# Kernel tuning notes

Measured on AMD Instinct MI355X. Metric: run time of the kernel, lower is better.

## Reference

```python
import jax, jax.numpy as jnp
import numpy as np

N_NODES = 50000

def _gcn_layer(x, src, dst, W, b, n_nodes):
    # x: [N, F_in]; src/dst: [E+N] (self-loops already appended)
    h = x @ W  # [N, F_out]
    deg = jax.ops.segment_sum(jnp.ones_like(dst, dtype=h.dtype), dst, num_segments=n_nodes)
    dinv = jnp.where(deg > 0, jax.lax.rsqrt(deg), 0.0)  # deg^{-1/2}
    norm = dinv[src] * dinv[dst]  # [E+N]
    msg = h[src] * norm[:, None]  # gather + scale
    out = jax.ops.segment_sum(msg, dst, num_segments=n_nodes)  # scatter-add
    return out + b

def setup_inputs() -> dict:
    key = jax.random.key(0)
    k1, k2, k3, k4 = jax.random.split(key, 4)
    d = 128
    E = 800000
    x = jax.random.normal(k1, (N_NODES, d), dtype=jnp.float32)
    edge_index = jax.random.randint(k2, (2, E), 0, N_NODES, dtype=jnp.int64)
    W1 = jax.random.normal(k3, (d, d), dtype=jnp.float32) / np.sqrt(d)
    b1 = jnp.zeros((d,), dtype=jnp.float32)
    W2 = jax.random.normal(k4, (d, d), dtype=jnp.float32) / np.sqrt(d)
    b2 = jnp.zeros((d,), dtype=jnp.float32)
    return {"x": x, "edge_index": edge_index, "W1": W1, "b1": b1, "W2": W2, "b2": b2}

def reference(x, edge_index, W1, b1, W2, b2):
    n = x.shape[0]
    loops = jnp.arange(n, dtype=edge_index.dtype)
    src = jnp.concatenate([edge_index[0], loops])  # add self-loops
    dst = jnp.concatenate([edge_index[1], loops])
    h = _gcn_layer(x, src, dst, W1, b1, n)
    h = jax.nn.relu(h)
    z = _gcn_layer(h, src, dst, W2, b2, n)
    return z
```

## Files before the change

### kernel.cpp

```cpp
#include <hip/hip_runtime.h>
#include <hip/hip_fp16.h>

#define NF 128
#define KC 64
#define NPART 4
#define NPMAX 12544

typedef _Float16 half8  __attribute__((ext_vector_type(8)));
typedef _Float16 half4v __attribute__((ext_vector_type(4)));
typedef float    floatx4 __attribute__((ext_vector_type(4)));

__global__ __launch_bounds__(512) void count2_k(
    const int* __restrict__ dst, unsigned char* __restrict__ pcnt,
    int E, int N, int Ec)
{
    __shared__ int lcnt[NPMAX];
    const int p = blockIdx.x & 3, c = blockIdx.x >> 2;
    const int Np = (N + 3) >> 2;
    const int lo = p * Np, hi = min(lo + Np, N);
    const int sz = hi - lo;
    for (int i = threadIdx.x; i < sz; i += 512) lcnt[i] = 0;
    __syncthreads();

    const int e0 = c * Ec, e1 = min(e0 + Ec, E);
    for (int e = e0 + (int)threadIdx.x * 4; e + 3 < e1; e += 512 * 4) {
        int4 d = *(const int4*)(dst + e);
        if (d.x >= lo && d.x < hi) atomicAdd(&lcnt[d.x - lo], 1);
        if (d.y >= lo && d.y < hi) atomicAdd(&lcnt[d.y - lo], 1);
        if (d.z >= lo && d.z < hi) atomicAdd(&lcnt[d.z - lo], 1);
        if (d.w >= lo && d.w < hi) atomicAdd(&lcnt[d.w - lo], 1);
    }
    int rem0 = e0 + ((e1 - e0) & ~3);
    for (int e = rem0 + (int)threadIdx.x; e < e1; e += 512) {
        int d = dst[e];
        if (d >= lo && d < hi) atomicAdd(&lcnt[d - lo], 1);
    }
    __syncthreads();
    for (int i = threadIdx.x; i < sz; i += 512)
        pcnt[(size_t)c * N + lo + i] = (unsigned char)lcnt[i];
}

__global__ __launch_bounds__(256) void pscan2_k(
    unsigned char* __restrict__ pcnt, float* __restrict__ dinv,
    int* __restrict__ rowptr, int* __restrict__ blocksum, int n, int N, int nb,
    const float* __restrict__ W1, const float* __restrict__ W2,
    __half* __restrict__ WT1, __half* __restrict__ WT2)
{
    if ((int)blockIdx.x >= nb) {
        int idx = ((int)blockIdx.x - nb) * 256 + threadIdx.x;
        const float* W = (idx < 16384) ? W1 : W2;
        __half* WT     = (idx < 16384) ? WT1 : WT2;
        int j = idx & 16383;
        int nn = j & 127, k = j >> 7;
        WT[nn * NF + k] = __float2half(W[k * NF + nn]);
        return;
    }
    __shared__ int sm[256];
    int tid = threadIdx.x;
    int bin = blockIdx.x * 256 + tid;
    int total = 0;
    if (bin < n) {
        #pragma unroll 4
        for (int c = 0; c < KC; c++) {
            size_t o = (size_t)c * N + bin;
            int v = pcnt[o];
            pcnt[o] = (unsigned char)total;
            total += v;
        }
        dinv[bin] = rsqrtf((float)total + 1.0f);
    }
    sm[tid] = total;
    __syncthreads();
    #pragma unroll
    for (int d = 1; d < 256; d <<= 1) {
        int t = (tid >= d) ? sm[tid - d] : 0;
        __syncthreads();
        sm[tid] += t;
        __syncthreads();
    }
    if (bin < n) rowptr[bin] = sm[tid] - total;
    if (tid == 255) blocksum[blockIdx.x] = sm[255];
}

template<bool F32IN>
__device__ __forceinline__ void gemm_body512(
    const void* __restrict__ Xv, const __half* __restrict__ WT,
    const float* __restrict__ dinv, __half* __restrict__ out, int M, int bid,
    __half (*wlds)[136])
{
    const int tid = threadIdx.x;
    {
        int r = tid >> 2;
        int c0 = (tid & 3) * 32;
        const half8* s = (const half8*)(WT + (size_t)r * NF + c0);
        half8* d = (half8*)&wlds[r][c0];
        #pragma unroll
        for (int j = 0; j < 4; j++) d[j] = s[j];
    }
    __syncthreads();

    const int wave = tid >> 6, lane = tid & 63;
    const int quad = lane >> 4, l15 = lane & 15;
    const int rowA = bid * 128 + wave * 16 + l15;
    const int rowc = (rowA < M) ? rowA : (M - 1);

    half8 afr[4];
    if (F32IN) {
        const float* X = (const float*)Xv;
        #pragma unroll
        for (int kc = 0; kc < 4; kc++) {
            const floatx4* p = (const floatx4*)(X + (size_t)rowc * NF + kc * 32 + quad * 8);
            floatx4 u = p[0], v = p[1];
            half8 a;
            a[0] = (_Float16)u[0]; a[1] = (_Float16)u[1];
            a[2] = (_Float16)u[2]; a[3] = (_Float16)u[3];
            a[4] = (_Float16)v[0]; a[5] = (_Float16)v[1];
            a[6] = (_Float16)v[2]; a[7] = (_Float16)v[3];
            afr[kc] = a;
        }
    } else {
        const __half* X = (const __half*)Xv;
        #pragma unroll
        for (int kc = 0; kc < 4; kc++)
            afr[kc] = *(const half8*)(X + (size_t)rowc * NF + kc * 32 + quad * 8);
    }

    floatx4 acc[8];
    #pragma unroll
    for (int ct = 0; ct < 8; ct++) { floatx4 z = {0.f, 0.f, 0.f, 0.f}; acc[ct] = z; }

    #pragma unroll
    for (int kc = 0; kc < 4; kc++) {
        #pragma unroll
        for (int ct = 0; ct < 8; ct++) {
            half8 b = *(const half8*)&wlds[ct * 16 + l15][kc * 32 + quad * 8];
            acc[ct] = __builtin_amdgcn_mfma_f32_16x16x32_f16(afr[kc], b, acc[ct], 0, 0, 0);
        }
    }

    const int orow0 = bid * 128 + wave * 16 + quad * 4;
    #pragma unroll
    for (int r = 0; r < 4; r++) {
        int orow = orow0 + r;
        if (orow < M) {
            float s = dinv[orow];
            #pragma unroll
            for (int ct = 0; ct < 8; ct++)
                out[(size_t)orow * NF + ct * 16 + l15] = __float2half(acc[ct][r] * s);
        }
    }
}

__global__ __launch_bounds__(512) void mid_k(
    const int* __restrict__ src, const int* __restrict__ dst,
    const int* __restrict__ rowptr, const unsigned char* __restrict__ coff,
    const int* __restrict__ blocksum, int* __restrict__ rowptr2,
    int* __restrict__ csr, int E, int N, int Ec, int nb,
    const float* __restrict__ X, const __half* __restrict__ WT,
    const float* __restrict__ dinv, __half* __restrict__ H, int GB2)
{
    __shared__ __align__(16) char smem[NPMAX * 4 + 1024];
    const int tid = threadIdx.x;
    if ((int)blockIdx.x < GB2) {
        gemm_body512<true>(X, WT, dinv, H, N, blockIdx.x, (__half(*)[136])smem);
        return;
    }
    int* lcur = (int*)smem;
    int* pref = (int*)(smem + NPMAX * 4);

    const int b = blockIdx.x - GB2;
    const int p = b & 3, c = b >> 2;
    const int Np = (N + 3) >> 2;
    const int lo = p * Np, hi = min(lo + Np, N);
    const int sz = hi - lo;

    int v = (tid < nb) ? blocksum[tid] : 0;
    if (tid < 256) pref[tid] = v;
    __syncthreads();
    #pragma unroll
    for (int d = 1; d < 256; d <<= 1) {
        int t = (tid < 256 && tid >= d) ? pref[tid - d] : 0;
        __syncthreads();
        if (tid < 256) pref[tid] += t;
        __syncthreads();
    }
    if (tid < 256) pref[tid] -= v;
    __syncthreads();

    for (int i = tid; i < sz; i += 512) {
        int bin = lo + i;
        int r = rowptr[bin] + pref[bin >> 8] + (int)coff[(size_t)c * N + bin];
        lcur[i] = r;
        if (c == 0) rowptr2[bin] = r;
    }
    if (c == 0 && p == 0 && tid == 0) rowptr2[N] = E;
    __syncthreads();

    const int e0 = c * Ec, e1 = min(e0 + Ec, E);
    for (int e = e0 + tid * 4; e + 3 < e1; e += 512 * 4) {
        int4 d = *(const int4*)(dst + e);
        int4 s = *(const int4*)(src + e);
        if (d.x >= lo && d.x < hi) csr[atomicAdd(&lcur[d.x - lo], 1)] = s.x;
        if (d.y >= lo && d.y < hi) csr[atomicAdd(&lcur[d.y - lo], 1)] = s.y;
        if (d.z >= lo && d.z < hi) csr[atomicAdd(&lcur[d.z - lo], 1)] = s.z;
        if (d.w >= lo && d.w < hi) csr[atomicAdd(&lcur[d.w - lo], 1)] = s.w;
    }
    int rem0 = e0 + ((e1 - e0) & ~3);
    for (int e = rem0 + tid; e < e1; e += 512) {
        int d = dst[e];
        if (d >= lo && d < hi) csr[atomicAdd(&lcur[d - lo], 1)] = src[e];
    }
}

__global__ __launch_bounds__(256) void bsort_k(
    const int* __restrict__ rowptr, int* __restrict__ csr, int n)
{
    int wave = threadIdx.x >> 6, lane = threadIdx.x & 63;
    int node = blockIdx.x * 4 + wave;
    if (node >= n) return;
    int base = rowptr[node], cnt = rowptr[node + 1] - base;
    for (int off = 0; off < cnt; off += 64) {
        int m = min(64, cnt - off);
        if (m <= 1) break;
        int v = (lane < m) ? csr[base + off + lane] : 0x7fffffff;
        #pragma unroll
        for (int k = 2; k <= 64; k <<= 1) {
            #pragma unroll
            for (int j = k >> 1; j >= 1; j >>= 1) {
                int pv = __shfl_xor(v, j, 64);
                bool up = ((lane & k) == 0);
                bool mn = (((lane & j) == 0) == up);
                v = mn ? min(v, pv) : max(v, pv);
            }
        }
        if (lane < m) csr[base + off + lane] = v;
    }
}

__device__ __forceinline__ void gather4s(
    const half4v* __restrict__ hs4, const int* __restrict__ csr,
    const int* __restrict__ rowptr, int node0, int n,
    int eg, int fl, int lane, floatx4 acc[4])
{
    int base[4], cc[4], rc[4], idx[4];
    int maxc = 0;
    #pragma unroll
    for (int k = 0; k < 4; k++) {
        int nd = node0 + k;
        int b0 = 0, c0 = 0;
        if (nd < n) { b0 = rowptr[nd]; c0 = rowptr[nd + 1] - b0; }
        base[k] = b0; rc[k] = c0; cc[k] = min(c0, 64);
        maxc = max(maxc, cc[k]);
    }
    #pragma unroll
    for (int k = 0; k < 4; k++)
        idx[k] = (lane < cc[k]) ? __builtin_nontemporal_load(&csr[base[k] + lane]) : 0;

    #pragma unroll
    for (int k = 0; k < 4; k++) { floatx4 z = {0.f, 0.f, 0.f, 0.f}; acc[k] = z; }

    if (eg == 0) {
        #pragma unroll
        for (int k = 0; k < 4; k++) {
            int nd = node0 + k;
            if (nd < n) {
                half4v s = hs4[(size_t)nd * 32 + fl];
                acc[k][0] += (float)s[0]; acc[k][1] += (float)s[1];
                acc[k][2] += (float)s[2]; acc[k][3] += (float)s[3];
            }
        }
    }

    const int rmax = (maxc + 1) >> 1;
    #pragma unroll 2
    for (int s = 0; s < rmax; s++) {
        const int e2 = s * 2;
        #pragma unroll
        for (int k = 0; k < 4; k++) {
            if (e2 < cc[k]) {
                int si = __shfl(idx[k], min(e2 + eg, cc[k] - 1), 64);
                half4v v = hs4[(size_t)si * 32 + fl];
                if (e2 + eg < cc[k]) {
                    acc[k][0] += (float)v[0]; acc[k][1] += (float)v[1];
                    acc[k][2] += (float)v[2]; acc[k][3] += (float)v[3];
                }
            }
        }
    }

    #pragma unroll
    for (int k = 0; k < 4; k++) {
        for (int off = 64; off < rc[k]; off += 64) {
            int m = min(64, rc[k] - off);
            int id2 = (lane < m) ? __builtin_nontemporal_load(&csr[base[k] + off + lane]) : 0;
            for (int j = 0; j < m; j += 2) {
                int si = __shfl(id2, min(j + eg, m - 1), 64);
                half4v v = hs4[(size_t)si * 32 + fl];
                if (j + eg < m) {
                    acc[k][0] += (float)v[0]; acc[k][1] += (float)v[1];
                    acc[k][2] += (float)v[2]; acc[k][3] += (float)v[3];
                }
            }
        }
    }

    #pragma unroll
    for (int k = 0; k < 4; k++) {
        #pragma unroll
        for (int q = 0; q < 4; q++)
            acc[k][q] += __shfl_xor(acc[k][q], 32, 64);
    }
}

__global__ __launch_bounds__(256) void aggmm_k(
    const __half* __restrict__ hs, const int* __restrict__ rowptr,
    const int* __restrict__ csr, const float* __restrict__ dinv,
    const float* __restrict__ bias, const __half* __restrict__ WT,
    __half* __restrict__ Hout, int n)
{
    __shared__ __half alds[16][136];
    const int tid = threadIdx.x;
    const int wave = tid >> 6, lane = tid & 63;
    const int eg = lane >> 5, fl = lane & 31;
    const int nb0 = blockIdx.x * 16;
    const int node0 = nb0 + wave * 4;

    floatx4 acc[4];
    gather4s((const half4v*)hs, csr, rowptr, node0, n, eg, fl, lane, acc);

    if (eg == 0) {
        #pragma unroll
        for (int k = 0; k < 4; k++) {
            int node = node0 + k;
            half4v h;
            if (node < n) {
                float dv = dinv[node];
                h[0] = (_Float16)fmaxf(dv * acc[k][0] + bias[fl * 4 + 0], 0.f);
                h[1] = (_Float16)fmaxf(dv * acc[k][1] + bias[fl * 4 + 1], 0.f);
                h[2] = (_Float16)fmaxf(dv * acc[k][2] + bias[fl * 4 + 2], 0.f);
                h[3] = (_Float16)fmaxf(dv * acc[k][3] + bias[fl * 4 + 3], 0.f);
            } else {
                h[0] = (_Float16)0.f; h[1] = (_Float16)0.f;
                h[2] = (_Float16)0.f; h[3] = (_Float16)0.f;
            }
            *(half4v*)&alds[wave * 4 + k][fl * 4] = h;
        }
    }
    __syncthreads();

    const int quad = lane >> 4, l15 = lane & 15;
    half8 afr[4];
    #pragma unroll
    for (int kc = 0; kc < 4; kc++)
        afr[kc] = *(const half8*)&alds[l15][kc * 32 + quad * 8];

    floatx4 acc0 = {0.f, 0.f, 0.f, 0.f};
    floatx4 acc1 = {0.f, 0.f, 0.f, 0.f};
    const int ct0 = wave * 2, ct1 = wave * 2 + 1;
    #pragma unroll
    for (int kc = 0; kc < 4; kc++) {
        half8 b0 = *(const half8*)(WT + (size_t)(ct0 * 16 + l15) * NF + kc * 32 + quad * 8);
        half8 b1 = *(const half8*)(WT + (size_t)(ct1 * 16 + l15) * NF + kc * 32 + quad * 8);
        acc0 = __builtin_amdgcn_mfma_f32_16x16x32_f16(afr[kc], b0, acc0, 0, 0, 0);
        acc1 = __builtin_amdgcn_mfma_f32_16x16x32_f16(afr[kc], b1, acc1, 0, 0, 0);
    }

    #pragma unroll
    for (int r = 0; r < 4; r++) {
        int row = quad * 4 + r;
        int node = nb0 + row;
        if (node < n) {
            float s = dinv[node];
            Hout[(size_t)node * NF + ct0 * 16 + l15] = __float2half(acc0[r] * s);
            Hout[(size_t)node * NF + ct1 * 16 + l15] = __float2half(acc1[r] * s);
        }
    }
}

__global__ __launch_bounds__(256) void agg4_k(
    const __half* __restrict__ hs, const int* __restrict__ rowptr,
    const int* __restrict__ csr, const float* __restrict__ dinv,
    const float* __restrict__ bias, float* __restrict__ outf, int n)
{
    const int tid = threadIdx.x;
    const int wave = tid >> 6, lane = tid & 63;
    const int eg = lane >> 5, fl = lane & 31;
    const int node0 = blockIdx.x * 16 + wave * 4;

    floatx4 acc[4];
    gather4s((const half4v*)hs, csr, rowptr, node0, n, eg, fl, lane, acc);

    if (eg == 0) {
        #pragma unroll
        for (int k = 0; k < 4; k++) {
            int node = node0 + k;
            if (node < n) {
                float dv = dinv[node];
                floatx4 w;
                w[0] = dv * acc[k][0] + bias[fl * 4 + 0];
                w[1] = dv * acc[k][1] + bias[fl * 4 + 1];
                w[2] = dv * acc[k][2] + bias[fl * 4 + 2];
                w[3] = dv * acc[k][3] + bias[fl * 4 + 3];
                *(floatx4*)(outf + (size_t)node * NF + fl * 4) = w;
            }
        }
    }
}


extern "C" void kernel_launch(void* const* d_in, const int* in_sizes, int n_in,
                              void* d_out, int out_size, void* d_ws, size_t ws_size,
                              hipStream_t stream) {
    const float* x  = (const float*)d_in[0];
    const int*   ei = (const int*)d_in[1];
    const float* W1 = (const float*)d_in[2];
    const float* b1 = (const float*)d_in[3];
    const float* W2 = (const float*)d_in[4];
    const float* b2 = (const float*)d_in[5];
    float* out = (float*)d_out;

    const int N = in_sizes[0] / NF;
    const int E = in_sizes[1] / 2;
    const int* src = ei;
    const int* dst = ei + E;

    char* ws = (char*)d_ws;
    size_t off = 0;
    auto alloc = [&](size_t bytes) {
        void* p = ws + off;
        off += bytes;
        off = (off + 63) & ~(size_t)63;
        return p;
    };
    unsigned char* pcnt = (unsigned char*)alloc((size_t)KC * N);
    int*    rowptr  = (int*)alloc((size_t)(N + 1) * 4);
    int*    rowptr2 = (int*)alloc((size_t)(N + 1) * 4);
    int*    csr     = (int*)alloc((size_t)E * 4);
    float*  dinv    = (float*)alloc((size_t)N * 4);
    int*    bsum    = (int*)alloc((size_t)256 * 4);
    __half* WT1     = (__half*)alloc((size_t)NF * NF * 2);
    __half* WT2     = (__half*)alloc((size_t)NF * NF * 2);
    __half* H16     = (__half*)alloc((size_t)N * NF * 2);
    __half* A16     = (__half*)alloc((size_t)N * NF * 2);

    int nb  = (N + 255) / 256;
    int Ec  = (((E + KC - 1) / KC) + 3) & ~3;
    int GB2 = (N + 127) / 128;
    int sb  = (N + 3) / 4;
    int fb  = (N + 15) / 16;

    count2_k<<<KC * NPART, 512, 0, stream>>>(dst, pcnt, E, N, Ec);
    pscan2_k<<<nb + 128, 256, 0, stream>>>(pcnt, dinv, rowptr, bsum, N, N, nb,
                                           W1, W2, WT1, WT2);
    mid_k<<<GB2 + KC * NPART, 512, 0, stream>>>(src, dst, rowptr, pcnt, bsum,
                                                rowptr2, csr, E, N, Ec, nb,
                                                x, WT1, dinv, H16, GB2);
    bsort_k<<<sb, 256, 0, stream>>>(rowptr2, csr, N);
    aggmm_k<<<fb, 256, 0, stream>>>(H16, rowptr2, csr, dinv, b1, WT2, A16, N);
    agg4_k<<<fb, 256, 0, stream>>>(A16, rowptr2, csr, dinv, b2, out, N);
}
```

Measured before the change: 233.3 us.

## Gather eight nodes per wave with batched loads in aggregation kernels

Each wave now aggregates eight destination nodes instead of four, and the blocks cover 32 nodes. The gather loop is split into phases: all index shuffles first, then all feature loads, then the accumulates, so more independent memory requests are in flight. The MFMA stage now handles two 16-row tiles per block, and launch bounds request 4 blocks per SIMD. The cost is higher register pressure and more divergence when node degrees vary within a wave, which could cut occupancy or force spills.

Measured after the change: 227.6 us. 2.4% less time.

```diff
diff --git a/kernel.cpp b/kernel.cpp
--- a/kernel.cpp
+++ b/kernel.cpp
@@ -237,15 +237,15 @@
     }
 }
 
-__device__ __forceinline__ void gather4s(
+__device__ __forceinline__ void gather8s(
     const half4v* __restrict__ hs4, const int* __restrict__ csr,
     const int* __restrict__ rowptr, int node0, int n,
-    int eg, int fl, int lane, floatx4 acc[4])
-{
-    int base[4], cc[4], rc[4], idx[4];
+    int eg, int fl, int lane, floatx4 acc[8])
+{
+    int base[8], cc[8], rc[8], idx[8];
     int maxc = 0;
     #pragma unroll
-    for (int k = 0; k < 4; k++) {
+    for (int k = 0; k < 8; k++) {
         int nd = node0 + k;
         int b0 = 0, c0 = 0;
         if (nd < n) { b0 = rowptr[nd]; c0 = rowptr[nd + 1] - b0; }
@@ -253,84 +253,96 @@
         maxc = max(maxc, cc[k]);
     }
     #pragma unroll
-    for (int k = 0; k < 4; k++)
+    for (int k = 0; k < 8; k++)
         idx[k] = (lane < cc[k]) ? __builtin_nontemporal_load(&csr[base[k] + lane]) : 0;
 
     #pragma unroll
-    for (int k = 0; k < 4; k++) { floatx4 z = {0.f, 0.f, 0.f, 0.f}; acc[k] = z; }
+    for (int k = 0; k < 8; k++) { floatx4 z = {0.f, 0.f, 0.f, 0.f}; acc[k] = z; }
 
     if (eg == 0) {
-        #pragma unroll
-        for (int k = 0; k < 4; k++) {
-            int nd = node0 + k;
-            if (nd < n) {
-                half4v s = hs4[(size_t)nd * 32 + fl];
-                acc[k][0] += (float)s[0]; acc[k][1] += (float)s[1];
-                acc[k][2] += (float)s[2]; acc[k][3] += (float)s[3];
+        half4v sv[8];
+        #pragma unroll
+        for (int k = 0; k < 8; k++) {
+            int nd = min(node0 + k, n - 1);
+            sv[k] = hs4[(size_t)nd * 32 + fl];
+        }
+        #pragma unroll
+        for (int k = 0; k < 8; k++) {
+            if (node0 + k < n) {
+                acc[k][0] += (float)sv[k][0]; acc[k][1] += (float)sv[k][1];
+                acc[k][2] += (float)sv[k][2]; acc[k][3] += (float)sv[k][3];
             }
         }
     }
 
     const int rmax = (maxc + 1) >> 1;
-    #pragma unroll 2
     for (int s = 0; s < rmax; s++) {
         const int e2 = s * 2;
-        #pragma unroll
-        for (int k = 0; k < 4; k++) {
-            if (e2 < cc[k]) {
-                int si = __shfl(idx[k], min(e2 + eg, cc[k] - 1), 64);
-                half4v v = hs4[(size_t)si * 32 + fl];
-                if (e2 + eg < cc[k]) {
-                    acc[k][0] += (float)v[0]; acc[k][1] += (float)v[1];
-                    acc[k][2] += (float)v[2]; acc[k][3] += (float)v[3];
+        int sidx[8];
+        half4v v[8];
+        #pragma unroll
+        for (int k = 0; k < 8; k++) {
+            int ec = min(e2 + eg, cc[k] - 1);
+            ec = (ec < 0) ? 0 : ec;
+            sidx[k] = __shfl(idx[k], ec, 64);
+        }
+        #pragma unroll
+        for (int k = 0; k < 8; k++)
+            v[k] = hs4[(size_t)sidx[k] * 32 + fl];
+        #pragma unroll
+        for (int k = 0; k < 8; k++) {
+            if (e2 + eg < cc[k]) {
+                acc[k][0] += (float)v[k][0]; acc[k][1] += (float)v[k][1];
+                acc[k][2] += (float)v[k][2]; acc[k][3] += (float)v[k][3];
+            }
+        }
+    }
+
+    #pragma unroll
+    for (int k = 0; k < 8; k++) {
+        if (rc[k] > 64) {
+            for (int off = 64; off < rc[k]; off += 64) {
+                int m = min(64, rc[k] - off);
+                int id2 = (lane < m) ? __builtin_nontemporal_load(&csr[base[k] + off + lane]) : 0;
+                for (int j = 0; j < m; j += 2) {
+                    int si = __shfl(id2, min(j + eg, m - 1), 64);
+                    half4v v = hs4[(size_t)si * 32 + fl];
+                    if (j + eg < m) {
+                        acc[k][0] += (float)v[0]; acc[k][1] += (float)v[1];
+                        acc[k][2] += (float)v[2]; acc[k][3] += (float)v[3];
+                    }
                 }
             }
         }
     }
 
     #pragma unroll
-    for (int k = 0; k < 4; k++) {
-        for (int off = 64; off < rc[k]; off += 64) {
-            int m = min(64, rc[k] - off);
-            int id2 = (lane < m) ? __builtin_nontemporal_load(&csr[base[k] + off + lane]) : 0;
-            for (int j = 0; j < m; j += 2) {
-                int si = __shfl(id2, min(j + eg, m - 1), 64);
-                half4v v = hs4[(size_t)si * 32 + fl];
-                if (j + eg < m) {
-                    acc[k][0] += (float)v[0]; acc[k][1] += (float)v[1];
-                    acc[k][2] += (float)v[2]; acc[k][3] += (float)v[3];
-                }
-            }
-        }
-    }
-
-    #pragma unroll
-    for (int k = 0; k < 4; k++) {
+    for (int k = 0; k < 8; k++) {
         #pragma unroll
         for (int q = 0; q < 4; q++)
             acc[k][q] += __shfl_xor(acc[k][q], 32, 64);
     }
 }
 
-__global__ __launch_bounds__(256) void aggmm_k(
+__global__ __launch_bounds__(256, 4) void aggmm_k(
     const __half* __restrict__ hs, const int* __restrict__ rowptr,
     const int* __restrict__ csr, const float* __restrict__ dinv,
     const float* __restrict__ bias, const __half* __restrict__ WT,
     __half* __restrict__ Hout, int n)
 {
-    __shared__ __half alds[16][136];
+    __shared__ __half alds[32][136];
     const int tid = threadIdx.x;
     const int wave = tid >> 6, lane = tid & 63;
     const int eg = lane >> 5, fl = lane & 31;
-    const int nb0 = blockIdx.x * 16;
-    const int node0 = nb0 + wave * 4;
-
-    floatx4 acc[4];
-    gather4s((const half4v*)hs, csr, rowptr, node0, n, eg, fl, lane, acc);
+    const int nb0 = blockIdx.x * 32;
+    const int node0 = nb0 + wave * 8;
+
+    floatx4 acc[8];
+    gather8s((const half4v*)hs, csr, rowptr, node0, n, eg, fl, lane, acc);
 
     if (eg == 0) {
         #pragma unroll
-        for (int k = 0; k < 4; k++) {
+        for (int k = 0; k < 8; k++) {
             int node = node0 + k;
             half4v h;
             if (node < n) {
@@ -343,41 +355,50 @@
                 h[0] = (_Float16)0.f; h[1] = (_Float16)0.f;
                 h[2] = (_Float16)0.f; h[3] = (_Float16)0.f;
             }
-            *(half4v*)&alds[wave * 4 + k][fl * 4] = h;
+            *(half4v*)&alds[wave * 8 + k][fl * 4] = h;
         }
     }
     __syncthreads();
 
     const int quad = lane >> 4, l15 = lane & 15;
-    half8 afr[4];
-    #pragma unroll
-    for (int kc = 0; kc < 4; kc++)
-        afr[kc] = *(const half8*)&alds[l15][kc * 32 + quad * 8];
-
-    floatx4 acc0 = {0.f, 0.f, 0.f, 0.f};
-    floatx4 acc1 = {0.f, 0.f, 0.f, 0.f};
+    half8 afr0[4], afr1[4];
+    #pragma unroll
+    for (int kc = 0; kc < 4; kc++) {
+        afr0[kc] = *(const half8*)&alds[l15][kc * 32 + quad * 8];
+        afr1[kc] = *(const half8*)&alds[16 + l15][kc * 32 + quad * 8];
+    }
+
+    floatx4 o00 = {0.f, 0.f, 0.f, 0.f}, o01 = {0.f, 0.f, 0.f, 0.f};
+    floatx4 o10 = {0.f, 0.f, 0.f, 0.f}, o11 = {0.f, 0.f, 0.f, 0.f};
     const int ct0 = wave * 2, ct1 = wave * 2 + 1;
     #pragma unroll
     for (int kc = 0; kc < 4; kc++) {
         half8 b0 = *(const half8*)(WT + (size_t)(ct0 * 16 + l15) * NF + kc * 32 + quad * 8);
         half8 b1 = *(const half8*)(WT + (size_t)(ct1 * 16 + l15) * NF + kc * 32 + quad * 8);
-        acc0 = __builtin_amdgcn_mfma_f32_16x16x32_f16(afr[kc], b0, acc0, 0, 0, 0);
-        acc1 = __builtin_amdgcn_mfma_f32_16x16x32_f16(afr[kc], b1, acc1, 0, 0, 0);
+        o00 = __builtin_amdgcn_mfma_f32_16x16x32_f16(afr0[kc], b0, o00, 0, 0, 0);
+        o01 = __builtin_amdgcn_mfma_f32_16x16x32_f16(afr0[kc], b1, o01, 0, 0, 0);
+        o10 = __builtin_amdgcn_mfma_f32_16x16x32_f16(afr1[kc], b0, o10, 0, 0, 0);
+        o11 = __builtin_amdgcn_mfma_f32_16x16x32_f16(afr1[kc], b1, o11, 0, 0, 0);
     }
 
     #pragma unroll
     for (int r = 0; r < 4; r++) {
-        int row = quad * 4 + r;
-        int node = nb0 + row;
-        if (node < n) {
-            float s = dinv[node];
-            Hout[(size_t)node * NF + ct0 * 16 + l15] = __float2half(acc0[r] * s);
-            Hout[(size_t)node * NF + ct1 * 16 + l15] = __float2half(acc1[r] * s);
-        }
-    }
-}
-
-__global__ __launch_bounds__(256) void agg4_k(
+        int n0 = nb0 + quad * 4 + r;
+        int n1 = n0 + 16;
+        if (n0 < n) {
+            float s = dinv[n0];
+            Hout[(size_t)n0 * NF + ct0 * 16 + l15] = __float2half(o00[r] * s);
+            Hout[(size_t)n0 * NF + ct1 * 16 + l15] = __float2half(o01[r] * s);
+        }
+        if (n1 < n) {
+            float s = dinv[n1];
+            Hout[(size_t)n1 * NF + ct0 * 16 + l15] = __float2half(o10[r] * s);
+            Hout[(size_t)n1 * NF + ct1 * 16 + l15] = __float2half(o11[r] * s);
+        }
+    }
+}
+
+__global__ __launch_bounds__(256, 4) void agg4_k(
     const __half* __restrict__ hs, const int* __restrict__ rowptr,
     const int* __restrict__ csr, const float* __restrict__ dinv,
     const float* __restrict__ bias, float* __restrict__ outf, int n)
@@ -385,14 +406,14 @@
     const int tid = threadIdx.x;
     const int wave = tid >> 6, lane = tid & 63;
     const int eg = lane >> 5, fl = lane & 31;
-    const int node0 = blockIdx.x * 16 + wave * 4;
-
-    floatx4 acc[4];
-    gather4s((const half4v*)hs, csr, rowptr, node0, n, eg, fl, lane, acc);
+    const int node0 = blockIdx.x * 32 + wave * 8;
+
+    floatx4 acc[8];
+    gather8s((const half4v*)hs, csr, rowptr, node0, n, eg, fl, lane, acc);
 
     if (eg == 0) {
         #pragma unroll
-        for (int k = 0; k < 4; k++) {
+        for (int k = 0; k < 8; k++) {
             int node = node0 + k;
             if (node < n) {
                 float dv = dinv[node];
@@ -447,7 +468,7 @@
     int Ec  = (((E + KC - 1) / KC) + 3) & ~3;
     int GB2 = (N + 127) / 128;
     int sb  = (N + 3) / 4;
-    int fb  = (N + 15) / 16;
+    int fb  = (N + 31) / 32;
 
     count2_k<<<KC * NPART, 512, 0, stream>>>(dst, pcnt, E, N, Ec);
     pscan2_k<<<nb + 128, 256, 0, stream>>>(pcnt, dinv, rowptr, bsum, N, N, nb,
```
